# Kernel optimization log

Measured on AMD Instinct MI355X. Metric: run time of the kernel, lower is better.

## Reference

```python
import jax, jax.numpy as jnp
import numpy as np

B, S, H = 1, 2048, 2048
I = 1408            # moe intermediate size
E = 16              # n_routed_experts
K = 6               # num_experts_per_tok
G = 4               # n_group
KG = 2              # topk_group
NSH = 2             # n_shared_experts -> shared intermediate = NSH*I
RSF = 2.5           # routed_scaling_factor
CAP = 2 * (B * S * K) // E


def setup_inputs() -> dict:
    key = jax.random.key(0)
    ks = jax.random.split(key, 9)
    sh = NSH * I
    s_h = 1.0 / np.sqrt(H).astype(np.float32)
    s_i = 1.0 / np.sqrt(I).astype(np.float32)
    s_s = 1.0 / np.sqrt(sh).astype(np.float32)
    return {
        "x": jax.random.normal(ks[0], (B, S, H), jnp.float32),
        "gate_w": jax.random.normal(ks[1], (E, H), jnp.float32) * s_h,
        "gate_bias": jnp.zeros((E,), jnp.float32),
        "w_gate": jax.random.normal(ks[2], (E, H, I), jnp.float32) * s_h,
        "w_up": jax.random.normal(ks[3], (E, H, I), jnp.float32) * s_h,
        "w_down": jax.random.normal(ks[4], (E, I, H), jnp.float32) * s_i,
        "ws_gate": jax.random.normal(ks[5], (H, sh), jnp.float32) * s_h,
        "ws_up": jax.random.normal(ks[6], (H, sh), jnp.float32) * s_h,
        "ws_down": jax.random.normal(ks[7], (sh, H), jnp.float32) * s_s,
    }


def _gate(x2d, gate_w, gate_bias):
    # MoEGate: fp32 linear -> sigmoid -> noaux_tc group-limited top-k
    logits = x2d.astype(jnp.float32) @ gate_w.astype(jnp.float32).T     # [T,E]
    scores = jax.nn.sigmoid(logits)
    scores_c = scores + gate_bias                                       # e_score_correction_bias
    T = scores.shape[0]
    gs = scores_c.reshape(T, G, E // G)
    top2, _ = jax.lax.top_k(gs, 2)
    group_scores = top2.sum(-1)                                         # [T,G] sum of top-2 per group
    _, gidx = jax.lax.top_k(group_scores, KG)                           # keep top KG groups
    gmask = jnp.zeros((T, G), scores.dtype).at[jnp.arange(T)[:, None], gidx].set(1.0)
    smask = jnp.repeat(gmask, E // G, axis=1)                           # [T,E]
    tmp = jnp.where(smask > 0, scores_c, 0.0)
    _, topk_idx = jax.lax.top_k(tmp, K)                                 # [T,K]
    topk_w = jnp.take_along_axis(scores, topk_idx, axis=1)              # weights from UNbiased scores
    topk_w = topk_w / (topk_w.sum(-1, keepdims=True) + 1e-20)           # norm_topk_prob
    topk_w = topk_w * RSF
    return topk_idx, topk_w


def reference(x, gate_w, gate_bias, w_gate, w_up, w_down, ws_gate, ws_up, ws_down):
    T = B * S
    x2d = x.reshape(T, H)
    topk_idx, topk_w = _gate(x2d, gate_w, gate_bias)

    # ---- dispatch: sort (token,k) assignments by expert id (grouped-GEMM layout) ----
    flat_e = topk_idx.reshape(-1)                       # [T*K]
    order = jnp.argsort(flat_e, stable=True)
    sorted_e = flat_e[order]
    counts = jnp.bincount(flat_e, length=E)             # batch_sizes per expert
    starts = jnp.concatenate([jnp.zeros((1,), counts.dtype), jnp.cumsum(counts)[:-1]])
    pos = jnp.arange(T * K) - starts[sorted_e]          # slot within expert bucket
    tok = order // K                                    # source token of each assignment
    buf = jnp.zeros((E, CAP, H), x.dtype).at[sorted_e, pos].set(x2d[tok], mode="drop")

    # ---- grouped SwiGLU expert FFN (gmm equivalent) ----
    g = jnp.einsum("ech,ehi->eci", buf, w_gate)
    u = jnp.einsum("ech,ehi->eci", buf, w_up)
    y_e = jnp.einsum("eci,eih->ech", jax.nn.silu(g) * u, w_down)

    # ---- combine: gather back, weight, scatter-add per token ----
    keep = (pos < CAP).astype(x.dtype)
    y_sorted = y_e[sorted_e, jnp.minimum(pos, CAP - 1)] * keep[:, None]
    w_flat = topk_w.reshape(-1)[order]
    y = jnp.zeros((T, H), x.dtype).at[tok].add(y_sorted * w_flat[:, None])

    # ---- shared experts (dense SwiGLU on all tokens) ----
    sg = x2d @ ws_gate
    su = x2d @ ws_up
    y = y + (jax.nn.silu(sg) * su) @ ws_down
    return y.reshape(B, S, H)
```

## Files before the change

### kernel.cpp

```cpp
#include <hip/hip_runtime.h>

typedef unsigned short u16;
typedef u16  u16x8 __attribute__((ext_vector_type(8)));
typedef u16  u16x4 __attribute__((ext_vector_type(4)));
typedef short s16x8 __attribute__((ext_vector_type(8)));
typedef float f32x4 __attribute__((ext_vector_type(4)));

static constexpr int TT   = 2048;
static constexpr int HD   = 2048;
static constexpr int ID   = 1408;
static constexpr int NE   = 16;
static constexpr int TOPK = 6;
static constexpr int CAPE = 1536;
static constexpr int SHD  = 2816;
static constexpr float RSF_ = 2.5f;
static constexpr int PGRID = 768;

__device__ __forceinline__ u16 f2b(float f) {
  unsigned int u = __builtin_bit_cast(unsigned int, f);
  unsigned int r = (u + 0x7FFFu + ((u >> 16) & 1u)) >> 16;
  return (u16)r;
}
__device__ __forceinline__ float b2f(u16 u) {
  unsigned int v = ((unsigned int)u) << 16;
  return __builtin_bit_cast(float, v);
}

__device__ __forceinline__ void gl_lds16(const u16* gp, u16* lp) {
  __builtin_amdgcn_global_load_lds(
      (const __attribute__((address_space(1))) void*)(unsigned long long)(const void*)gp,
      (__attribute__((address_space(3))) void*)(unsigned int)(unsigned long long)(void*)lp,
      16, 0, 0);
}

__device__ __forceinline__ void seq_map(int idx, int mtiles, int ntiles,
                                        int& bx, int& by, int& e) {
  bx = idx % mtiles;
  int tq = idx / mtiles;
  by = tq % ntiles;
  e  = tq / ntiles;
}

__global__ __launch_bounds__(256) void k_cvt(const float* __restrict__ in, u16* __restrict__ out) {
  size_t i = (size_t)blockIdx.x * 256 + threadIdx.x;
  const float4* p = (const float4*)in;
  float4 v0 = p[i * 2], v1 = p[i * 2 + 1];
  u16x8 o = { f2b(v0.x), f2b(v0.y), f2b(v0.z), f2b(v0.w),
              f2b(v1.x), f2b(v1.y), f2b(v1.z), f2b(v1.w) };
  *(u16x8*)(out + i * 8) = o;
}

__global__ __launch_bounds__(64) void k_init(int* c) {
  if (threadIdx.x < 16) c[threadIdx.x] = 0;
}

__global__ __launch_bounds__(256) void k_gate2(const float* __restrict__ x,
    const float* __restrict__ gw, const float* __restrict__ gb,
    int* __restrict__ topk_idx, float* __restrict__ topk_w) {
  const int t = threadIdx.x;
  const int tok0 = blockIdx.x * 8;
  const int i  = t >> 5;
  const int sub = t & 31;
  const int e  = sub & 15;
  const int kh = sub >> 4;
  const float4* xr = (const float4*)(x + (size_t)(tok0 + i) * HD) + kh * (HD / 8);
  const float4* wr = (const float4*)(gw + (size_t)e * HD) + kh * (HD / 8);
  float acc = 0.f;
  #pragma unroll 8
  for (int k = 0; k < HD / 8; ++k) {
    float4 a = xr[k], b = wr[k];
    acc += a.x * b.x + a.y * b.y;
    acc += a.z * b.z + a.w * b.w;
  }
  acc += __shfl_down(acc, 16);
  __shared__ float lg[8][16];
  if (sub < 16) lg[i][e] = acc;
  __syncthreads();
  if (t >= 8) return;
  const int tok = tok0 + t;
  float s[NE], sc[NE];
  #pragma unroll
  for (int ee = 0; ee < NE; ++ee) {
    s[ee]  = 1.f / (1.f + expf(-lg[t][ee]));
    sc[ee] = s[ee] + gb[ee];
  }
  float gs[4];
  #pragma unroll
  for (int g = 0; g < 4; ++g) {
    float m1 = -1e30f, m2 = -1e30f;
    #pragma unroll
    for (int j = 0; j < 4; ++j) {
      float v = sc[g * 4 + j];
      if (v > m1) { m2 = m1; m1 = v; } else if (v > m2) m2 = v;
    }
    gs[g] = m1 + m2;
  }
  int g0 = 0;
  #pragma unroll
  for (int g = 1; g < 4; ++g) if (gs[g] > gs[g0]) g0 = g;
  int g1 = -1; float g1v = -1e30f;
  #pragma unroll
  for (int g = 0; g < 4; ++g) {
    if (g == g0) continue;
    if (g1 < 0 || gs[g] > g1v) { g1 = g; g1v = gs[g]; }
  }
  float tmp[NE];
  #pragma unroll
  for (int ee = 0; ee < NE; ++ee) {
    int g = ee >> 2;
    tmp[ee] = (g == g0 || g == g1) ? sc[ee] : 0.0f;
  }
  unsigned used = 0;
  float wsum = 0.f;
  int idxs[TOPK]; float wv[TOPK];
  #pragma unroll
  for (int k = 0; k < TOPK; ++k) {
    int best = -1; float bv = -2e30f;
    #pragma unroll
    for (int ee = 0; ee < NE; ++ee) {
      bool ok = (((used >> ee) & 1u) == 0u) && (tmp[ee] > bv);
      if (ok) { bv = tmp[ee]; best = ee; }
    }
    used |= 1u << best;
    float sv = 0.f;
    #pragma unroll
    for (int ee = 0; ee < NE; ++ee) if (ee == best) sv = s[ee];
    idxs[k] = best; wv[k] = sv; wsum += sv;
  }
  float scale = RSF_ / (wsum + 1e-20f);
  #pragma unroll
  for (int k = 0; k < TOPK; ++k) {
    topk_idx[tok * TOPK + k] = idxs[k];
    topk_w[tok * TOPK + k]   = wv[k] * scale;
  }
}

__global__ __launch_bounds__(256) void k_count_pos(const int* __restrict__ topk_idx,
    int* __restrict__ rowidx, int* __restrict__ tok_of_row, int* __restrict__ counts) {
  const int e = blockIdx.x, t = threadIdx.x;
  __shared__ int pref[256];
  const int t0 = t * 8;
  int c = 0;
  for (int tt = t0; tt < t0 + 8; ++tt)
    for (int k = 0; k < TOPK; ++k) c += (topk_idx[tt * TOPK + k] == e) ? 1 : 0;
  pref[t] = c;
  __syncthreads();
  for (int off = 1; off < 256; off <<= 1) {
    int v = (t >= off) ? pref[t - off] : 0;
    __syncthreads();
    pref[t] += v;
    __syncthreads();
  }
  int run = pref[t] - c;
  if (t == 255) counts[e] = (pref[255] < CAPE) ? pref[255] : CAPE;
  for (int tt = t0; tt < t0 + 8; ++tt)
    for (int k = 0; k < TOPK; ++k)
      if (topk_idx[tt * TOPK + k] == e) {
        if (run < CAPE) {
          rowidx[tt * TOPK + k] = e * CAPE + run;
          tok_of_row[e * CAPE + run] = tt;
        } else {
          rowidx[tt * TOPK + k] = -1;
        }
        ++run;
      }
}

__global__ __launch_bounds__(256) void k_transpose_cvt(const float* __restrict__ in,
    u16* __restrict__ out, int R, int Cc, long zin, long zout) {
  __shared__ float tile[64][65];
  const float* src = in + (size_t)blockIdx.z * zin;
  u16* dst = out + (size_t)blockIdx.z * zout;
  const int r0 = blockIdx.x * 64, c0 = blockIdx.y * 64, t = threadIdx.x;
  #pragma unroll
  for (int i = 0; i < 4; ++i) {
    int c = t + 256 * i;
    int r = c >> 4, cg = (c & 15) << 2;
    float4 v = *(const float4*)(src + (size_t)(r0 + r) * Cc + c0 + cg);
    tile[r][cg + 0] = v.x; tile[r][cg + 1] = v.y;
    tile[r][cg + 2] = v.z; tile[r][cg + 3] = v.w;
  }
  __syncthreads();
  #pragma unroll
  for (int i = 0; i < 4; ++i) {
    int c = t + 256 * i;
    int oc = c >> 4, og = (c & 15) << 2;
    u16x4 w;
    #pragma unroll
    for (int j = 0; j < 4; ++j) w[j] = f2b(tile[og + j][oc]);
    *(u16x4*)(dst + (size_t)(c0 + oc) * R + r0 + og) = w;
  }
}

__global__ __launch_bounds__(256, 4) void k_pdual(
    const u16* __restrict__ A, const u16* __restrict__ B0, const u16* __restrict__ B1,
    u16* __restrict__ C, const int* __restrict__ row_map, const int* __restrict__ counts,
    int Mfixed, int K, int lda, int ldc, long b_stride, int row_cap,
    int mtiles, int ntiles, int nexp, int* __restrict__ counter) {
  const int t = threadIdx.x;
  const int l = t & 63, w = t >> 6;
  const int wm = (w >> 1) * 64, wn = (w & 1) * 32;
  const int l15 = l & 15, g0 = l >> 4;

  __shared__ __align__(16) u16 As[2][128 * 32];
  __shared__ __align__(16) u16 B0s[2][64 * 32];
  __shared__ __align__(16) u16 B1s[2][64 * 32];
  __shared__ int s_tile;

  int aoff[4], boff[2];
  #pragma unroll
  for (int i = 0; i < 4; ++i) {
    int rA = wm + i * 16 + l15;
    aoff[i] = rA * 64 + ((g0 ^ ((rA >> 1) & 3)) << 4);
  }
  #pragma unroll
  for (int i = 0; i < 2; ++i) {
    int rB = wn + i * 16 + l15;
    boff[i] = rB * 64 + ((g0 ^ ((rB >> 1) & 3)) << 4);
  }

  const int ntot = mtiles * ntiles * nexp;
  const int nk = K >> 5;
  const int cl = l15, rw = g0 * 4;

  for (;;) {
    if (t == 0) s_tile = atomicAdd(counter, 1);
    __syncthreads();
    int idx = s_tile;
    __syncthreads();
    if (idx >= ntot) break;
    int bx, by, e;
    seq_map(idx, mtiles, ntiles, bx, by, e);
    const int cnt = counts ? counts[e] : Mfixed;
    const int M_e = counts ? (cnt < row_cap ? cnt : row_cap) : Mfixed;
    const int m0 = bx * 128;
    if (m0 >= M_e) continue;
    const int n0 = by * 64;
    const int row_base = counts ? e * row_cap : 0;
    const u16* B0e = B0 + (size_t)e * b_stride;
    const u16* B1e = B1 + (size_t)e * b_stride;

    const u16 *ap[2], *b0p, *b1p;
    int loffA[2], loffB;
    #pragma unroll
    for (int i = 0; i < 2; ++i) {
      int c = t + 256 * i;
      int row = c >> 2, g = c & 3;
      int kg = g ^ ((row >> 1) & 3);
      loffA[i] = c * 8;
      int rg = m0 + row; if (rg > M_e - 1) rg = M_e - 1;
      int arow = row_map ? row_map[row_base + rg] : row_base + rg;
      ap[i] = A + (size_t)arow * lda + kg * 8;
    }
    {
      int row = t >> 2, g = t & 3;
      int kg = g ^ ((row >> 1) & 3);
      loffB = t * 8;
      b0p = B0e + (size_t)(n0 + row) * K + kg * 8;
      b1p = B1e + (size_t)(n0 + row) * K + kg * 8;
    }

    f32x4 accg[4][2], accu[4][2];
    #pragma unroll
    for (int m = 0; m < 4; ++m)
      #pragma unroll
      for (int n = 0; n < 2; ++n) { accg[m][n] = f32x4{0,0,0,0}; accu[m][n] = f32x4{0,0,0,0}; }

    #pragma unroll
    for (int i = 0; i < 2; ++i) { gl_lds16(ap[i], &As[0][loffA[i]]); ap[i] += 32; }
    gl_lds16(b0p, &B0s[0][loffB]); b0p += 32;
    gl_lds16(b1p, &B1s[0][loffB]); b1p += 32;
    __syncthreads();
    int cur = 0;
    for (int ks = 0; ks < nk; ++ks) {
      if (ks + 1 < nk) {
        #pragma unroll
        for (int i = 0; i < 2; ++i) { gl_lds16(ap[i], &As[cur ^ 1][loffA[i]]); ap[i] += 32; }
        gl_lds16(b0p, &B0s[cur ^ 1][loffB]); b0p += 32;
        gl_lds16(b1p, &B1s[cur ^ 1][loffB]); b1p += 32;
      }
      s16x8 af[4], bf0[2], bf1[2];
      #pragma unroll
      for (int i = 0; i < 4; ++i)
        af[i] = __builtin_bit_cast(s16x8, *(const u16x8*)((const char*)As[cur] + aoff[i]));
      #pragma unroll
      for (int i = 0; i < 2; ++i) {
        bf0[i] = __builtin_bit_cast(s16x8, *(const u16x8*)((const char*)B0s[cur] + boff[i]));
        bf1[i] = __builtin_bit_cast(s16x8, *(const u16x8*)((const char*)B1s[cur] + boff[i]));
      }
      #pragma unroll
      for (int m = 0; m < 4; ++m)
        #pragma unroll
        for (int n = 0; n < 2; ++n) {
          accg[m][n] = __builtin_amdgcn_mfma_f32_16x16x32_bf16(af[m], bf0[n], accg[m][n], 0, 0, 0);
          accu[m][n] = __builtin_amdgcn_mfma_f32_16x16x32_bf16(af[m], bf1[n], accu[m][n], 0, 0, 0);
        }
      __syncthreads();
      cur ^= 1;
    }

    #pragma unroll
    for (int m = 0; m < 4; ++m) {
      #pragma unroll
      for (int n = 0; n < 2; ++n) {
        f32x4 vg = accg[m][n], vu = accu[m][n];
        int gr0 = m0 + wm + m * 16 + rw;
        int gc  = n0 + wn + n * 16 + cl;
        #pragma unroll
        for (int j = 0; j < 4; ++j) {
          int rr = gr0 + j;
          if (rr < M_e) {
            float gf = vg[j];
            float act = gf / (1.f + __expf(-gf)) * vu[j];
            C[(size_t)(row_base + rr) * ldc + gc] = f2b(act);
          }
        }
      }
    }
  }
}

template <int EPI>
__global__ __launch_bounds__(256, 4) void k_psing(
    const u16* __restrict__ A, const u16* __restrict__ Bt, void* __restrict__ Cptr,
    const int* __restrict__ counts, int Mfixed, int K, int lda, int ldc,
    long b_stride, int row_cap, int mtiles, int ntiles, int nexp,
    int* __restrict__ counter) {
  const int t = threadIdx.x;
  const int l = t & 63, w = t >> 6;
  const int wm = (w >> 1) * 64, wn = (w & 1) * 64;
  const int l15 = l & 15, g0 = l >> 4;

  __shared__ __align__(16) u16 As[2][128 * 32];
  __shared__ __align__(16) u16 Bs[2][128 * 32];
  __shared__ int s_tile;

  int aoff[4], boff[4];
  #pragma unroll
  for (int i = 0; i < 4; ++i) {
    int rA = wm + i * 16 + l15;
    int rB = wn + i * 16 + l15;
    aoff[i] = rA * 64 + ((g0 ^ ((rA >> 1) & 3)) << 4);
    boff[i] = rB * 64 + ((g0 ^ ((rB >> 1) & 3)) << 4);
  }

  const int ntot = mtiles * ntiles * nexp;
  const int nk = K >> 5;
  const int cl = l15, rw = g0 * 4;

  for (;;) {
    if (t == 0) s_tile = atomicAdd(counter, 1);
    __syncthreads();
    int idx = s_tile;
    __syncthreads();
    if (idx >= ntot) break;
    int bx, by, e;
    seq_map(idx, mtiles, ntiles, bx, by, e);
    const int cnt = counts ? counts[e] : Mfixed;
    const int M_e = counts ? (cnt < row_cap ? cnt : row_cap) : Mfixed;
    const int m0 = bx * 128;
    if (m0 >= M_e) continue;
    const int n0 = by * 128;
    const int row_base = counts ? e * row_cap : 0;
    const u16* Bte = Bt + (size_t)e * b_stride;

    const u16 *ap[2], *bp[2];
    int loff[2];
    #pragma unroll
    for (int i = 0; i < 2; ++i) {
      int c = t + 256 * i;
      int row = c >> 2, g = c & 3;
      int kg = g ^ ((row >> 1) & 3);
      loff[i] = c * 8;
      int rg = m0 + row; if (rg > M_e - 1) rg = M_e - 1;
      ap[i] = A + (size_t)(row_base + rg) * lda + kg * 8;
      bp[i] = Bte + (size_t)(n0 + row) * K + kg * 8;
    }

    f32x4 acc[4][4];
    #pragma unroll
    for (int m = 0; m < 4; ++m)
      #pragma unroll
      for (int n = 0; n < 4; ++n) acc[m][n] = f32x4{0, 0, 0, 0};

    #pragma unroll
    for (int i = 0; i < 2; ++i) {
      gl_lds16(ap[i], &As[0][loff[i]]); ap[i] += 32;
      gl_lds16(bp[i], &Bs[0][loff[i]]); bp[i] += 32;
    }
    __syncthreads();
    int cur = 0;
    for (int ks = 0; ks < nk; ++ks) {
      if (ks + 1 < nk) {
        #pragma unroll
        for (int i = 0; i < 2; ++i) {
          gl_lds16(ap[i], &As[cur ^ 1][loff[i]]); ap[i] += 32;
          gl_lds16(bp[i], &Bs[cur ^ 1][loff[i]]); bp[i] += 32;
        }
      }
      s16x8 af[4], bfr[4];
      #pragma unroll
      for (int i = 0; i < 4; ++i) {
        af[i]  = __builtin_bit_cast(s16x8, *(const u16x8*)((const char*)As[cur] + aoff[i]));
        bfr[i] = __builtin_bit_cast(s16x8, *(const u16x8*)((const char*)Bs[cur] + boff[i]));
      }
      #pragma unroll
      for (int m = 0; m < 4; ++m)
        #pragma unroll
        for (int n = 0; n < 4; ++n)
          acc[m][n] = __builtin_amdgcn_mfma_f32_16x16x32_bf16(af[m], bfr[n], acc[m][n], 0, 0, 0);
      __syncthreads();
      cur ^= 1;
    }

    #pragma unroll
    for (int m = 0; m < 4; ++m) {
      #pragma unroll
      for (int n = 0; n < 4; ++n) {
        f32x4 v = acc[m][n];
        int gr0 = m0 + wm + m * 16 + rw;
        int gc  = n0 + wn + n * 16 + cl;
        #pragma unroll
        for (int j = 0; j < 4; ++j) {
          int rr = gr0 + j;
          if (rr < M_e) {
            size_t ci = (size_t)(row_base + rr) * ldc + gc;
            if (EPI == 1) ((float*)Cptr)[ci] = v[j];
            else          ((u16*)Cptr)[ci]   = f2b(v[j]);
          }
        }
      }
    }
  }
}

__global__ __launch_bounds__(256) void k_combine(const u16* __restrict__ down,
    const int* __restrict__ rowidx, const float* __restrict__ tw,
    float* __restrict__ out) {
  const int t = blockIdx.x, l = threadIdx.x;
  __shared__ int rid[TOPK];
  __shared__ float wk[TOPK];
  if (l < TOPK) { rid[l] = rowidx[t * TOPK + l]; wk[l] = tw[t * TOPK + l]; }
  __syncthreads();
  const int h0 = l * 8;
  float* op = out + (size_t)t * HD + h0;
  float4 o0 = *(float4*)op, o1 = *(float4*)(op + 4);
  float a[8] = { o0.x, o0.y, o0.z, o0.w, o1.x, o1.y, o1.z, o1.w };
  #pragma unroll
  for (int k = 0; k < TOPK; ++k) {
    int r = rid[k];
    if (r < 0) continue;
    float wkk = wk[k];
    u16x8 v = *(const u16x8*)(down + (size_t)r * HD + h0);
    #pragma unroll
    for (int j = 0; j < 8; ++j) a[j] += wkk * b2f(v[j]);
  }
  o0 = make_float4(a[0], a[1], a[2], a[3]);
  o1 = make_float4(a[4], a[5], a[6], a[7]);
  *(float4*)op = o0;
  *(float4*)(op + 4) = o1;
}

__global__ __launch_bounds__(256) void k_sentinel(float* o, int n) {
  int i = blockIdx.x * 256 + threadIdx.x;
  if (i < n) o[i] = 12345.0f;
}

extern "C" void kernel_launch(void* const* d_in, const int* in_sizes, int n_in,
                              void* d_out, int out_size, void* d_ws, size_t ws_size,
                              hipStream_t stream) {
  const float* x       = (const float*)d_in[0];
  const float* gate_w  = (const float*)d_in[1];
  const float* gate_b  = (const float*)d_in[2];
  const float* w_gate  = (const float*)d_in[3];
  const float* w_up    = (const float*)d_in[4];
  const float* w_down  = (const float*)d_in[5];
  const float* ws_gate = (const float*)d_in[6];
  const float* ws_up   = (const float*)d_in[7];
  const float* ws_down = (const float*)d_in[8];
  float* out = (float*)d_out;

  char* base = (char*)d_ws;
  char* p = base;
  auto alloc = [&](size_t bytes) -> char* {
    char* r = p;
    p += (bytes + 255) & ~(size_t)255;
    return r;
  };
  u16* slotA = (u16*)alloc((size_t)NE * ID * HD * 2);
  u16* slotB = (u16*)alloc((size_t)NE * CAPE * HD * 2);
  u16* xb    = (u16*)alloc((size_t)TT * HD * 2);
  u16* gbuf  = (u16*)alloc((size_t)NE * CAPE * ID * 2);
  u16* swTg  = (u16*)alloc((size_t)SHD * HD * 2);
  u16* swTu  = (u16*)alloc((size_t)SHD * HD * 2);
  u16* sgb   = (u16*)alloc((size_t)TT * SHD * 2);
  int*   tidx  = (int*)alloc((size_t)TT * TOPK * 4);
  float* twv   = (float*)alloc((size_t)TT * TOPK * 4);
  int*   ridx  = (int*)alloc((size_t)TT * TOPK * 4);
  int*   torow = (int*)alloc((size_t)NE * CAPE * 4);
  int*   cnts  = (int*)alloc(64);
  int*   ctrs  = (int*)alloc(64);
  u16* wTg = slotA;
  u16* wTu = slotB;
  u16* wTd = slotA;
  u16* dbuf = slotB;

  if ((size_t)(p - base) > ws_size) {
    k_sentinel<<<dim3((out_size + 255) / 256), dim3(256), 0, stream>>>(out, out_size);
    return;
  }

  dim3 b256(256);

  k_cvt<<<dim3((TT * HD) / (8 * 256)), b256, 0, stream>>>(x, xb);
  k_init<<<dim3(1), dim3(64), 0, stream>>>(ctrs);
  k_gate2<<<dim3(TT / 8), b256, 0, stream>>>(x, gate_w, gate_b, tidx, twv);
  k_count_pos<<<dim3(NE), b256, 0, stream>>>(tidx, ridx, torow, cnts);

  k_transpose_cvt<<<dim3(HD / 64, ID / 64, NE), b256, 0, stream>>>(
      w_gate, wTg, HD, ID, (long)HD * ID, (long)ID * HD);
  k_transpose_cvt<<<dim3(HD / 64, ID / 64, NE), b256, 0, stream>>>(
      w_up, wTu, HD, ID, (long)HD * ID, (long)ID * HD);
  k_pdual<<<dim3(PGRID), b256, 0, stream>>>(
      xb, wTg, wTu, gbuf, torow, cnts, 0, HD, HD, ID, (long)ID * HD, CAPE,
      CAPE / 128, ID / 64, NE, ctrs + 0);
  k_transpose_cvt<<<dim3(ID / 64, HD / 64, NE), b256, 0, stream>>>(
      w_down, wTd, ID, HD, (long)ID * HD, (long)HD * ID);
  k_psing<0><<<dim3(PGRID), b256, 0, stream>>>(
      gbuf, wTd, dbuf, cnts, 0, ID, ID, HD, (long)HD * ID, CAPE,
      CAPE / 128, HD / 128, NE, ctrs + 1);

  k_transpose_cvt<<<dim3(HD / 64, SHD / 64, 1), b256, 0, stream>>>(ws_gate, swTg, HD, SHD, 0, 0);
  k_transpose_cvt<<<dim3(HD / 64, SHD / 64, 1), b256, 0, stream>>>(ws_up, swTu, HD, SHD, 0, 0);
  k_pdual<<<dim3(PGRID), b256, 0, stream>>>(
      xb, swTg, swTu, sgb, nullptr, nullptr, TT, HD, HD, SHD, 0, 0,
      TT / 128, SHD / 64, 1, ctrs + 2);
  k_transpose_cvt<<<dim3(SHD / 64, HD / 64, 1), b256, 0, stream>>>(ws_down, swTg, SHD, HD, 0, 0);
  k_psing<1><<<dim3(PGRID), b256, 0, stream>>>(
      sgb, swTg, out, nullptr, TT, SHD, SHD, HD, 0, 0,
      TT / 128, HD / 128, 1, ctrs + 3);

  k_combine<<<dim3(TT), b256, 0, stream>>>(dbuf, ridx, twv, out);
}
```

Baseline: 756.8 us.

## Replace persistent down-proj GEMM with one-shot grid kernel using K=64 tiles

The two down-projection GEMMs switch from a persistent atomic-counter tile scheduler to a plain 3D grid launch. Block indices are remapped so consecutive tiles land on the same XCD, and each k-step stages 64 instead of 32 elements of K with an 8-way XOR swizzle. This removes per-tile atomics and barriers and halves the number of k-loop iterations and syncs, at the cost of twice the LDS per block and lower occupancy. PGRID for the remaining persistent dual GEMMs is raised from 768 to 1024.

```diff
diff --git a/kernel.cpp b/kernel.cpp
--- a/kernel.cpp
+++ b/kernel.cpp
@@ -14,7 +14,7 @@
 static constexpr int CAPE = 1536;
 static constexpr int SHD  = 2816;
 static constexpr float RSF_ = 2.5f;
-static constexpr int PGRID = 768;
+static constexpr int PGRID = 1024;
 
 __device__ __forceinline__ u16 f2b(float f) {
   unsigned int u = __builtin_bit_cast(unsigned int, f);
@@ -321,113 +321,116 @@
 }
 
 template <int EPI>
-__global__ __launch_bounds__(256, 4) void k_psing(
+__global__ __launch_bounds__(256) void k_gemm3(
     const u16* __restrict__ A, const u16* __restrict__ Bt, void* __restrict__ Cptr,
     const int* __restrict__ counts, int Mfixed, int K, int lda, int ldc,
-    long b_stride, int row_cap, int mtiles, int ntiles, int nexp,
-    int* __restrict__ counter) {
+    long b_stride, int row_cap) {
+  unsigned gx = gridDim.x, gy = gridDim.y, gz = gridDim.z;
+  unsigned F = (blockIdx.z * gy + blockIdx.y) * gx + blockIdx.x;
+  unsigned Nn = gx * gy * gz;
+  unsigned q = Nn >> 3, r = Nn & 7;
+  unsigned xcd = F & 7, pos = F >> 3;
+  unsigned wi = (xcd < r) ? xcd * (q + 1) + pos
+                          : r * (q + 1) + (xcd - r) * q + pos;
+  unsigned bx = wi % gx, tq = wi / gx;
+  unsigned by = tq % gy, bz = tq / gy;
+
+  const int e = bz;
+  const int cnt = counts ? counts[e] : Mfixed;
+  const int M_e = counts ? (cnt < row_cap ? cnt : row_cap) : Mfixed;
+  const int m0 = bx * 128;
+  if (m0 >= M_e) return;
+  const int n0 = by * 128;
+  const int row_base = counts ? e * row_cap : 0;
+  const u16* Bte = Bt + (size_t)e * b_stride;
+
+  __shared__ __align__(16) u16 As[2][128 * 64];
+  __shared__ __align__(16) u16 Bs[2][128 * 64];
+
   const int t = threadIdx.x;
   const int l = t & 63, w = t >> 6;
   const int wm = (w >> 1) * 64, wn = (w & 1) * 64;
+
+  const u16 *ap[4], *bp[4];
+  int loff[4];
+  #pragma unroll
+  for (int i = 0; i < 4; ++i) {
+    int c = t + 256 * i;
+    int row = c >> 3, pphys = c & 7;
+    int kc = pphys ^ (row & 7);
+    loff[i] = c * 8;
+    int rg = m0 + row; if (rg > M_e - 1) rg = M_e - 1;
+    ap[i] = A + (size_t)(row_base + rg) * lda + kc * 8;
+    bp[i] = Bte + (size_t)(n0 + row) * K + kc * 8;
+  }
+
+  f32x4 acc[4][4];
+  #pragma unroll
+  for (int m = 0; m < 4; ++m)
+    #pragma unroll
+    for (int n = 0; n < 4; ++n) acc[m][n] = f32x4{0, 0, 0, 0};
+
   const int l15 = l & 15, g0 = l >> 4;
-
-  __shared__ __align__(16) u16 As[2][128 * 32];
-  __shared__ __align__(16) u16 Bs[2][128 * 32];
-  __shared__ int s_tile;
-
-  int aoff[4], boff[4];
+  int aoff[2][4], boff[2][4];
+  #pragma unroll
+  for (int s = 0; s < 2; ++s)
+    #pragma unroll
+    for (int i = 0; i < 4; ++i) {
+      int rA = wm + i * 16 + l15;
+      int rB = wn + i * 16 + l15;
+      aoff[s][i] = rA * 128 + ((((s << 2) | g0) ^ (rA & 7)) << 4);
+      boff[s][i] = rB * 128 + ((((s << 2) | g0) ^ (rB & 7)) << 4);
+    }
+
+  const int nk = K >> 6;
   #pragma unroll
   for (int i = 0; i < 4; ++i) {
-    int rA = wm + i * 16 + l15;
-    int rB = wn + i * 16 + l15;
-    aoff[i] = rA * 64 + ((g0 ^ ((rA >> 1) & 3)) << 4);
-    boff[i] = rB * 64 + ((g0 ^ ((rB >> 1) & 3)) << 4);
-  }
-
-  const int ntot = mtiles * ntiles * nexp;
-  const int nk = K >> 5;
-  const int cl = l15, rw = g0 * 4;
-
-  for (;;) {
-    if (t == 0) s_tile = atomicAdd(counter, 1);
-    __syncthreads();
-    int idx = s_tile;
-    __syncthreads();
-    if (idx >= ntot) break;
-    int bx, by, e;
-    seq_map(idx, mtiles, ntiles, bx, by, e);
-    const int cnt = counts ? counts[e] : Mfixed;
-    const int M_e = counts ? (cnt < row_cap ? cnt : row_cap) : Mfixed;
-    const int m0 = bx * 128;
-    if (m0 >= M_e) continue;
-    const int n0 = by * 128;
-    const int row_base = counts ? e * row_cap : 0;
-    const u16* Bte = Bt + (size_t)e * b_stride;
-
-    const u16 *ap[2], *bp[2];
-    int loff[2];
-    #pragma unroll
-    for (int i = 0; i < 2; ++i) {
-      int c = t + 256 * i;
-      int row = c >> 2, g = c & 3;
-      int kg = g ^ ((row >> 1) & 3);
-      loff[i] = c * 8;
-      int rg = m0 + row; if (rg > M_e - 1) rg = M_e - 1;
-      ap[i] = A + (size_t)(row_base + rg) * lda + kg * 8;
-      bp[i] = Bte + (size_t)(n0 + row) * K + kg * 8;
-    }
-
-    f32x4 acc[4][4];
-    #pragma unroll
-    for (int m = 0; m < 4; ++m)
-      #pragma unroll
-      for (int n = 0; n < 4; ++n) acc[m][n] = f32x4{0, 0, 0, 0};
-
-    #pragma unroll
-    for (int i = 0; i < 2; ++i) {
-      gl_lds16(ap[i], &As[0][loff[i]]); ap[i] += 32;
-      gl_lds16(bp[i], &Bs[0][loff[i]]); bp[i] += 32;
-    }
-    __syncthreads();
-    int cur = 0;
-    for (int ks = 0; ks < nk; ++ks) {
-      if (ks + 1 < nk) {
-        #pragma unroll
-        for (int i = 0; i < 2; ++i) {
-          gl_lds16(ap[i], &As[cur ^ 1][loff[i]]); ap[i] += 32;
-          gl_lds16(bp[i], &Bs[cur ^ 1][loff[i]]); bp[i] += 32;
-        }
-      }
+    gl_lds16(ap[i], &As[0][loff[i]]); ap[i] += 64;
+    gl_lds16(bp[i], &Bs[0][loff[i]]); bp[i] += 64;
+  }
+  __syncthreads();
+  int cur = 0;
+  for (int ks = 0; ks < nk; ++ks) {
+    if (ks + 1 < nk) {
+      #pragma unroll
+      for (int i = 0; i < 4; ++i) {
+        gl_lds16(ap[i], &As[cur ^ 1][loff[i]]); ap[i] += 64;
+        gl_lds16(bp[i], &Bs[cur ^ 1][loff[i]]); bp[i] += 64;
+      }
+    }
+    #pragma unroll
+    for (int s = 0; s < 2; ++s) {
       s16x8 af[4], bfr[4];
       #pragma unroll
       for (int i = 0; i < 4; ++i) {
-        af[i]  = __builtin_bit_cast(s16x8, *(const u16x8*)((const char*)As[cur] + aoff[i]));
-        bfr[i] = __builtin_bit_cast(s16x8, *(const u16x8*)((const char*)Bs[cur] + boff[i]));
+        af[i]  = __builtin_bit_cast(s16x8, *(const u16x8*)((const char*)As[cur] + aoff[s][i]));
+        bfr[i] = __builtin_bit_cast(s16x8, *(const u16x8*)((const char*)Bs[cur] + boff[s][i]));
       }
       #pragma unroll
       for (int m = 0; m < 4; ++m)
         #pragma unroll
         for (int n = 0; n < 4; ++n)
           acc[m][n] = __builtin_amdgcn_mfma_f32_16x16x32_bf16(af[m], bfr[n], acc[m][n], 0, 0, 0);
-      __syncthreads();
-      cur ^= 1;
-    }
-
-    #pragma unroll
-    for (int m = 0; m < 4; ++m) {
-      #pragma unroll
-      for (int n = 0; n < 4; ++n) {
-        f32x4 v = acc[m][n];
-        int gr0 = m0 + wm + m * 16 + rw;
-        int gc  = n0 + wn + n * 16 + cl;
-        #pragma unroll
-        for (int j = 0; j < 4; ++j) {
-          int rr = gr0 + j;
-          if (rr < M_e) {
-            size_t ci = (size_t)(row_base + rr) * ldc + gc;
-            if (EPI == 1) ((float*)Cptr)[ci] = v[j];
-            else          ((u16*)Cptr)[ci]   = f2b(v[j]);
-          }
+    }
+    __syncthreads();
+    cur ^= 1;
+  }
+
+  const int cl = l15, rw = g0 * 4;
+  #pragma unroll
+  for (int m = 0; m < 4; ++m) {
+    #pragma unroll
+    for (int n = 0; n < 4; ++n) {
+      f32x4 v = acc[m][n];
+      int gr0 = m0 + wm + m * 16 + rw;
+      int gc  = n0 + wn + n * 16 + cl;
+      #pragma unroll
+      for (int j = 0; j < 4; ++j) {
+        int rr = gr0 + j;
+        if (rr < M_e) {
+          size_t ci = (size_t)(row_base + rr) * ldc + gc;
+          if (EPI == 1) ((float*)Cptr)[ci] = v[j];
+          else          ((u16*)Cptr)[ci]   = f2b(v[j]);
         }
       }
     }
@@ -526,19 +529,17 @@
       CAPE / 128, ID / 64, NE, ctrs + 0);
   k_transpose_cvt<<<dim3(ID / 64, HD / 64, NE), b256, 0, stream>>>(
       w_down, wTd, ID, HD, (long)ID * HD, (long)HD * ID);
-  k_psing<0><<<dim3(PGRID), b256, 0, stream>>>(
-      gbuf, wTd, dbuf, cnts, 0, ID, ID, HD, (long)HD * ID, CAPE,
-      CAPE / 128, HD / 128, NE, ctrs + 1);
+  k_gemm3<0><<<dim3(CAPE / 128, HD / 128, NE), b256, 0, stream>>>(
+      gbuf, wTd, dbuf, cnts, 0, ID, ID, HD, (long)HD * ID, CAPE);
 
   k_transpose_cvt<<<dim3(HD / 64, SHD / 64, 1), b256, 0, stream>>>(ws_gate, swTg, HD, SHD, 0, 0);
   k_transpose_cvt<<<dim3(HD / 64, SHD / 64, 1), b256, 0, stream>>>(ws_up, swTu, HD, SHD, 0, 0);
   k_pdual<<<dim3(PGRID), b256, 0, stream>>>(
       xb, swTg, swTu, sgb, nullptr, nullptr, TT, HD, HD, SHD, 0, 0,
-      TT / 128, SHD / 64, 1, ctrs + 2);
+      TT / 128, SHD / 64, 1, ctrs + 1);
   k_transpose_cvt<<<dim3(SHD / 64, HD / 64, 1), b256, 0, stream>>>(ws_down, swTg, SHD, HD, 0, 0);
-  k_psing<1><<<dim3(PGRID), b256, 0, stream>>>(
-      sgb, swTg, out, nullptr, TT, SHD, SHD, HD, 0, 0,
-      TT / 128, HD / 128, 1, ctrs + 3);
+  k_gemm3<1><<<dim3(TT / 128, HD / 128, 1), b256, 0, stream>>>(
+      sgb, swTg, out, nullptr, TT, SHD, SHD, HD, 0, 0);
 
   k_combine<<<dim3(TT), b256, 0, stream>>>(dbuf, ridx, twv, out);
 }
```

Measured after the change: 723.5 us. 1.05x faster.

## Replace persistent atomic-scheduled single GEMM with XCD-swizzled static grid launch

Applied to the files above, without the earlier changes.

The down-projection GEMMs (routed and shared) drop the persistent atomic work-queue kernel and use a plain 3D grid with one tile per block. A block-index remap groups consecutive tiles onto the same XCD to improve L2 reuse, and empty expert tiles exit early. The persistent grid size for the remaining dual GEMM kernels rises from 768 to 1024 blocks. This trades the atomic-counter and extra barrier overhead for launching many blocks that exit immediately on empty expert tiles.

```diff
diff --git a/kernel.cpp b/kernel.cpp
--- a/kernel.cpp
+++ b/kernel.cpp
@@ -14,7 +14,7 @@
 static constexpr int CAPE = 1536;
 static constexpr int SHD  = 2816;
 static constexpr float RSF_ = 2.5f;
-static constexpr int PGRID = 768;
+static constexpr int PGRID = 1024;
 
 __device__ __forceinline__ u16 f2b(float f) {
   unsigned int u = __builtin_bit_cast(unsigned int, f);
@@ -321,20 +321,56 @@
 }
 
 template <int EPI>
-__global__ __launch_bounds__(256, 4) void k_psing(
+__global__ __launch_bounds__(256, 4) void k_gemm5(
     const u16* __restrict__ A, const u16* __restrict__ Bt, void* __restrict__ Cptr,
     const int* __restrict__ counts, int Mfixed, int K, int lda, int ldc,
-    long b_stride, int row_cap, int mtiles, int ntiles, int nexp,
-    int* __restrict__ counter) {
+    long b_stride, int row_cap) {
+  unsigned gx = gridDim.x, gy = gridDim.y, gz = gridDim.z;
+  unsigned F = (blockIdx.z * gy + blockIdx.y) * gx + blockIdx.x;
+  unsigned Nn = gx * gy * gz;
+  unsigned q = Nn >> 3, r = Nn & 7;
+  unsigned xcd = F & 7, pos = F >> 3;
+  unsigned wi = (xcd < r) ? xcd * (q + 1) + pos
+                          : r * (q + 1) + (xcd - r) * q + pos;
+  unsigned bx = wi % gx, tq = wi / gx;
+  unsigned by = tq % gy, bz = tq / gy;
+
+  const int e = bz;
+  const int cnt = counts ? counts[e] : Mfixed;
+  const int M_e = counts ? (cnt < row_cap ? cnt : row_cap) : Mfixed;
+  const int m0 = bx * 128;
+  if (m0 >= M_e) return;
+  const int n0 = by * 128;
+  const int row_base = counts ? e * row_cap : 0;
+  const u16* Bte = Bt + (size_t)e * b_stride;
+
+  __shared__ __align__(16) u16 As[2][128 * 32];
+  __shared__ __align__(16) u16 Bs[2][128 * 32];
+
   const int t = threadIdx.x;
   const int l = t & 63, w = t >> 6;
   const int wm = (w >> 1) * 64, wn = (w & 1) * 64;
+
+  const u16 *ap[2], *bp[2];
+  int loff[2];
+  #pragma unroll
+  for (int i = 0; i < 2; ++i) {
+    int c = t + 256 * i;
+    int row = c >> 2, g = c & 3;
+    int kg = g ^ ((row >> 1) & 3);
+    loff[i] = c * 8;
+    int rg = m0 + row; if (rg > M_e - 1) rg = M_e - 1;
+    ap[i] = A + (size_t)(row_base + rg) * lda + kg * 8;
+    bp[i] = Bte + (size_t)(n0 + row) * K + kg * 8;
+  }
+
+  f32x4 acc[4][4];
+  #pragma unroll
+  for (int m = 0; m < 4; ++m)
+    #pragma unroll
+    for (int n = 0; n < 4; ++n) acc[m][n] = f32x4{0, 0, 0, 0};
+
   const int l15 = l & 15, g0 = l >> 4;
-
-  __shared__ __align__(16) u16 As[2][128 * 32];
-  __shared__ __align__(16) u16 Bs[2][128 * 32];
-  __shared__ int s_tile;
-
   int aoff[4], boff[4];
   #pragma unroll
   for (int i = 0; i < 4; ++i) {
@@ -344,90 +380,52 @@
     boff[i] = rB * 64 + ((g0 ^ ((rB >> 1) & 3)) << 4);
   }
 
-  const int ntot = mtiles * ntiles * nexp;
   const int nk = K >> 5;
+  #pragma unroll
+  for (int i = 0; i < 2; ++i) {
+    gl_lds16(ap[i], &As[0][loff[i]]); ap[i] += 32;
+    gl_lds16(bp[i], &Bs[0][loff[i]]); bp[i] += 32;
+  }
+  __syncthreads();
+  int cur = 0;
+  for (int ks = 0; ks < nk; ++ks) {
+    if (ks + 1 < nk) {
+      #pragma unroll
+      for (int i = 0; i < 2; ++i) {
+        gl_lds16(ap[i], &As[cur ^ 1][loff[i]]); ap[i] += 32;
+        gl_lds16(bp[i], &Bs[cur ^ 1][loff[i]]); bp[i] += 32;
+      }
+    }
+    s16x8 af[4], bfr[4];
+    #pragma unroll
+    for (int i = 0; i < 4; ++i) {
+      af[i]  = __builtin_bit_cast(s16x8, *(const u16x8*)((const char*)As[cur] + aoff[i]));
+      bfr[i] = __builtin_bit_cast(s16x8, *(const u16x8*)((const char*)Bs[cur] + boff[i]));
+    }
+    #pragma unroll
+    for (int m = 0; m < 4; ++m)
+      #pragma unroll
+      for (int n = 0; n < 4; ++n)
+        acc[m][n] = __builtin_amdgcn_mfma_f32_16x16x32_bf16(af[m], bfr[n], acc[m][n], 0, 0, 0);
+    __syncthreads();
+    cur ^= 1;
+  }
+
   const int cl = l15, rw = g0 * 4;
-
-  for (;;) {
-    if (t == 0) s_tile = atomicAdd(counter, 1);
-    __syncthreads();
-    int idx = s_tile;
-    __syncthreads();
-    if (idx >= ntot) break;
-    int bx, by, e;
-    seq_map(idx, mtiles, ntiles, bx, by, e);
-    const int cnt = counts ? counts[e] : Mfixed;
-    const int M_e = counts ? (cnt < row_cap ? cnt : row_cap) : Mfixed;
-    const int m0 = bx * 128;
-    if (m0 >= M_e) continue;
-    const int n0 = by * 128;
-    const int row_base = counts ? e * row_cap : 0;
-    const u16* Bte = Bt + (size_t)e * b_stride;
-
-    const u16 *ap[2], *bp[2];
-    int loff[2];
-    #pragma unroll
-    for (int i = 0; i < 2; ++i) {
-      int c = t + 256 * i;
-      int row = c >> 2, g = c & 3;
-      int kg = g ^ ((row >> 1) & 3);
-      loff[i] = c * 8;
-      int rg = m0 + row; if (rg > M_e - 1) rg = M_e - 1;
-      ap[i] = A + (size_t)(row_base + rg) * lda + kg * 8;
-      bp[i] = Bte + (size_t)(n0 + row) * K + kg * 8;
-    }
-
-    f32x4 acc[4][4];
-    #pragma unroll
-    for (int m = 0; m < 4; ++m)
-      #pragma unroll
-      for (int n = 0; n < 4; ++n) acc[m][n] = f32x4{0, 0, 0, 0};
-
-    #pragma unroll
-    for (int i = 0; i < 2; ++i) {
-      gl_lds16(ap[i], &As[0][loff[i]]); ap[i] += 32;
-      gl_lds16(bp[i], &Bs[0][loff[i]]); bp[i] += 32;
-    }
-    __syncthreads();
-    int cur = 0;
-    for (int ks = 0; ks < nk; ++ks) {
-      if (ks + 1 < nk) {
-        #pragma unroll
-        for (int i = 0; i < 2; ++i) {
-          gl_lds16(ap[i], &As[cur ^ 1][loff[i]]); ap[i] += 32;
-          gl_lds16(bp[i], &Bs[cur ^ 1][loff[i]]); bp[i] += 32;
-        }
-      }
-      s16x8 af[4], bfr[4];
-      #pragma unroll
-      for (int i = 0; i < 4; ++i) {
-        af[i]  = __builtin_bit_cast(s16x8, *(const u16x8*)((const char*)As[cur] + aoff[i]));
-        bfr[i] = __builtin_bit_cast(s16x8, *(const u16x8*)((const char*)Bs[cur] + boff[i]));
-      }
-      #pragma unroll
-      for (int m = 0; m < 4; ++m)
-        #pragma unroll
-        for (int n = 0; n < 4; ++n)
-          acc[m][n] = __builtin_amdgcn_mfma_f32_16x16x32_bf16(af[m], bfr[n], acc[m][n], 0, 0, 0);
-      __syncthreads();
-      cur ^= 1;
-    }
-
-    #pragma unroll
-    for (int m = 0; m < 4; ++m) {
-      #pragma unroll
-      for (int n = 0; n < 4; ++n) {
-        f32x4 v = acc[m][n];
-        int gr0 = m0 + wm + m * 16 + rw;
-        int gc  = n0 + wn + n * 16 + cl;
-        #pragma unroll
-        for (int j = 0; j < 4; ++j) {
-          int rr = gr0 + j;
-          if (rr < M_e) {
-            size_t ci = (size_t)(row_base + rr) * ldc + gc;
-            if (EPI == 1) ((float*)Cptr)[ci] = v[j];
-            else          ((u16*)Cptr)[ci]   = f2b(v[j]);
-          }
+  #pragma unroll
+  for (int m = 0; m < 4; ++m) {
+    #pragma unroll
+    for (int n = 0; n < 4; ++n) {
+      f32x4 v = acc[m][n];
+      int gr0 = m0 + wm + m * 16 + rw;
+      int gc  = n0 + wn + n * 16 + cl;
+      #pragma unroll
+      for (int j = 0; j < 4; ++j) {
+        int rr = gr0 + j;
+        if (rr < M_e) {
+          size_t ci = (size_t)(row_base + rr) * ldc + gc;
+          if (EPI == 1) ((float*)Cptr)[ci] = v[j];
+          else          ((u16*)Cptr)[ci]   = f2b(v[j]);
         }
       }
     }
@@ -526,19 +524,17 @@
       CAPE / 128, ID / 64, NE, ctrs + 0);
   k_transpose_cvt<<<dim3(ID / 64, HD / 64, NE), b256, 0, stream>>>(
       w_down, wTd, ID, HD, (long)ID * HD, (long)HD * ID);
-  k_psing<0><<<dim3(PGRID), b256, 0, stream>>>(
-      gbuf, wTd, dbuf, cnts, 0, ID, ID, HD, (long)HD * ID, CAPE,
-      CAPE / 128, HD / 128, NE, ctrs + 1);
+  k_gemm5<0><<<dim3(CAPE / 128, HD / 128, NE), b256, 0, stream>>>(
+      gbuf, wTd, dbuf, cnts, 0, ID, ID, HD, (long)HD * ID, CAPE);
 
   k_transpose_cvt<<<dim3(HD / 64, SHD / 64, 1), b256, 0, stream>>>(ws_gate, swTg, HD, SHD, 0, 0);
   k_transpose_cvt<<<dim3(HD / 64, SHD / 64, 1), b256, 0, stream>>>(ws_up, swTu, HD, SHD, 0, 0);
   k_pdual<<<dim3(PGRID), b256, 0, stream>>>(
       xb, swTg, swTu, sgb, nullptr, nullptr, TT, HD, HD, SHD, 0, 0,
-      TT / 128, SHD / 64, 1, ctrs + 2);
+      TT / 128, SHD / 64, 1, ctrs + 1);
   k_transpose_cvt<<<dim3(SHD / 64, HD / 64, 1), b256, 0, stream>>>(ws_down, swTg, SHD, HD, 0, 0);
-  k_psing<1><<<dim3(PGRID), b256, 0, stream>>>(
-      sgb, swTg, out, nullptr, TT, SHD, SHD, HD, 0, 0,
-      TT / 128, HD / 128, 1, ctrs + 3);
+  k_gemm5<1><<<dim3(TT / 128, HD / 128, 1), b256, 0, stream>>>(
+      sgb, swTg, out, nullptr, TT, SHD, SHD, HD, 0, 0);
 
   k_combine<<<dim3(TT), b256, 0, stream>>>(dbuf, ridx, twv, out);
 }
```

New measurement: 726.4 us. 4.0% less time.
